# Performance work log

Hardware: AMD Instinct MI355X
Metric: run time of the kernel (lower is better)

## Reference

```python
import math
import jax, jax.numpy as jnp
import numpy as np

B, T, C = 1, 2048, 2048
H, G, D = 16, 4, 128          # n_head, n_query_groups, head_size; C == H*D
Q_PER_KV = H // G
EPS = 1e-5


def _apply_rope_interleaved(x, cos, sin):
    # x: [B, T, h, D]; cos/sin: [T, D//2]; interleaved (GPT-J) style pairs
    x1 = x[..., 0::2]
    x2 = x[..., 1::2]
    c = cos[None, :, None, :]
    s = sin[None, :, None, :]
    o1 = x1 * c - x2 * s
    o2 = x1 * s + x2 * c
    return jnp.stack([o1, o2], axis=-1).reshape(x.shape)


def setup_inputs() -> dict:
    key = jax.random.key(0)
    k0, k1, k2, k3 = jax.random.split(key, 4)
    x = jax.random.normal(k0, (B, T, C), jnp.float32)
    # rotary cache (standard theta=10000)
    inv_freq = 1.0 / (10000.0 ** (np.arange(0, D, 2, dtype=np.float64) / D))
    ang = np.outer(np.arange(T, dtype=np.float64), inv_freq)
    cos = jnp.asarray(np.cos(ang), jnp.float32)
    sin = jnp.asarray(np.sin(ang), jnp.float32)
    # RetNet per-head decay mask: D[h,i,j] = gamma_h^(i-j) for i>=j else 0
    gammas = 1.0 - 2.0 ** (-5.0 - np.arange(H, dtype=np.float64))
    i = np.arange(T)[:, None]
    j = np.arange(T)[None, :]
    diff = np.maximum(i - j, 0).astype(np.float64)
    m = np.where(i >= j, gammas[:, None, None] ** diff[None], 0.0)
    mask = jnp.asarray(m, jnp.float32)
    std = 0.02
    W_reten = jax.random.normal(k1, (C, (H + 2 * G) * D), jnp.float32) * std
    W_gate = jax.random.normal(k2, (C, C), jnp.float32) * std
    W_proj = jax.random.normal(k3, (C, C), jnp.float32) * std
    return {"x": x, "cos": cos, "sin": sin, "mask": mask,
            "W_reten": W_reten, "W_gate": W_gate, "W_proj": W_proj,
            "max_seq_length": T}


def reference(x, cos, sin, mask, W_reten, W_gate, W_proj, max_seq_length):
    # fused qkv projection, grouped-query layout
    qkv = (x @ W_reten).reshape(B, T, G, Q_PER_KV + 2, D)
    q = qkv[..., :Q_PER_KV, :].reshape(B, T, H, D)
    k = qkv[..., Q_PER_KV:Q_PER_KV + 1, :].reshape(B, T, G, D)
    v = qkv[..., Q_PER_KV + 1:, :].reshape(B, T, G, D)
    q = _apply_rope_interleaved(q, cos, sin)
    k = _apply_rope_interleaved(k, cos, sin)
    # [B, h, T, D]
    q = q.transpose(0, 2, 1, 3)
    k = jnp.repeat(k.transpose(0, 2, 1, 3), Q_PER_KV, axis=1)
    v = jnp.repeat(v.transpose(0, 2, 1, 3), Q_PER_KV, axis=1)
    # parallel retention: masked (decay) scores, no softmax
    scale = 1.0 / math.sqrt(D)
    qk = jnp.einsum('bhtd,bhsd->bhts', q, k) * scale
    qk = qk * mask[None]
    y = jnp.einsum('bhts,bhsd->bhtd', qk, v)
    # group norm = RMSNorm (no weight) over head_size
    y = y.transpose(0, 2, 1, 3)  # [B, T, H, D]
    y = y * jax.lax.rsqrt(jnp.mean(y * y, axis=-1, keepdims=True) + EPS)
    y = y.reshape(B, T, C)
    g = jax.nn.silu(x @ W_gate)
    return (g * y) @ W_proj
```

## Files before the change

### kernel.cpp

```cpp
#include <hip/hip_runtime.h>
#include <hip/hip_bf16.h>
#include <cstdint>
#include <cstddef>

typedef __bf16 bf16x8 __attribute__((ext_vector_type(8)));
typedef __bf16 bf16x4 __attribute__((ext_vector_type(4)));
typedef __bf16 bf16x2 __attribute__((ext_vector_type(2)));
typedef float  f32x4  __attribute__((ext_vector_type(4)));
typedef float  f32x2  __attribute__((ext_vector_type(2)));

#define T_SEQ 2048
#define CDIM  2048
#define NH    16
#define NG    4
#define DH    128
#define NCHUNK 32

__device__ __forceinline__ void gl_lds16(const __bf16* g, __bf16* l) {
  __builtin_amdgcn_global_load_lds(
      (const __attribute__((address_space(1))) void*)g,
      (__attribute__((address_space(3))) void*)l, 16, 0, 0);
}

__global__ __launch_bounds__(256) void pre_kernel(
    const float* __restrict__ x, const float* __restrict__ Wr,
    const float* __restrict__ Wg, const float* __restrict__ Wp,
    __bf16* __restrict__ xb, __bf16* __restrict__ wtb, __bf16* __restrict__ wpb) {
  __shared__ __bf16 tile[64][68];
  int bid = blockIdx.x;
  int tid = threadIdx.x;
  if (bid < 2048) {
    size_t i = ((size_t)bid * 256 + tid) * 8;
    f32x4 a = *(const f32x4*)(x + i);
    f32x4 b = *(const f32x4*)(x + i + 4);
    bf16x8 o;
#pragma unroll
    for (int j = 0; j < 4; ++j) { o[j] = (__bf16)a[j]; o[4 + j] = (__bf16)b[j]; }
    *(bf16x8*)(xb + i) = o;
    return;
  }
  int rel = bid - 2048;
  const float* W; __bf16* Wt; int N;
  if (rel < 1536)      { W = Wr; Wt = wtb;                        N = 3072; }
  else if (rel < 2560) { W = Wg; Wt = wtb + (size_t)3072 * CDIM;  N = 2048; rel -= 1536; }
  else                 { W = Wp; Wt = wpb;                        N = 2048; rel -= 2560; }
  const int K = 2048;
  int k0 = (rel & 31) * 64, n0 = (rel >> 5) * 64;
  int c4 = (tid & 15) * 4, r = tid >> 4;
#pragma unroll
  for (int rr = 0; rr < 4; ++rr) {
    int row = r + rr * 16;
    f32x4 v = *(const f32x4*)(W + (size_t)(k0 + row) * N + n0 + c4);
#pragma unroll
    for (int j = 0; j < 4; ++j) tile[row][c4 + j] = (__bf16)v[j];
  }
  __syncthreads();
  int n = tid >> 2, seg = tid & 3;
  __bf16 vals[16];
#pragma unroll
  for (int j = 0; j < 16; ++j) vals[j] = tile[seg * 16 + j][n];
  __bf16* dst = Wt + (size_t)(n0 + n) * K + k0 + seg * 16;
  *(bf16x8*)(dst)     = *(bf16x8*)(&vals[0]);
  *(bf16x8*)(dst + 8) = *(bf16x8*)(&vals[8]);
}

__global__ __launch_bounds__(256) void uscan_kernel(const __bf16* __restrict__ vtb,
                                                    const __bf16* __restrict__ ktb,
                                                    __bf16* __restrict__ St) {
  int bid = blockIdx.x;
  int h = bid >> 4, m = (bid >> 1) & 7, half = bid & 1;
  int g = h >> 2;
  int tid = threadIdx.x, w = tid >> 6, l = tid & 63, lr = l & 15, lg = l >> 4;
  int jf = half * 4 + w;
  float l2g = log2f(1.0f - exp2f(-5.0f - (float)h));
  float ginv = exp2f(-l2g);
  float df   = exp2f(l2g * 64.0f);
  float wk[2];
#pragma unroll
  for (int kk = 0; kk < 2; ++kk) wk[kk] = exp2f(l2g * (float)(64 - (kk * 32 + lg * 8)));
  const __bf16* vrow = vtb + ((size_t)g * DH + m * 16 + lr) * T_SEQ;
  const __bf16* krow = ktb + ((size_t)g * DH + jf * 16 + lr) * T_SEQ;
  f32x4 S = {0.f, 0.f, 0.f, 0.f};
  for (int c = 0; c < NCHUNK; ++c) {
    f32x4 u = {0.f, 0.f, 0.f, 0.f};
#pragma unroll
    for (int kk = 0; kk < 2; ++kk) {
      int j0 = c * 64 + kk * 32 + lg * 8;
      bf16x8 av = *(const bf16x8*)(vrow + j0);
      bf16x8 bv = *(const bf16x8*)(krow + j0);
      bf16x8 aw;
      float wj = wk[kk];
#pragma unroll
      for (int jj = 0; jj < 8; ++jj) { aw[jj] = (__bf16)((float)av[jj] * wj); wj *= ginv; }
      u = __builtin_amdgcn_mfma_f32_16x16x32_bf16(aw, bv, u, 0, 0, 0);
    }
    __bf16* out = St + ((size_t)(h * NCHUNK + c) * 128 + m * 16 + lg * 4) * 128 + jf * 16 + lr;
#pragma unroll
    for (int r = 0; r < 4; ++r) out[r * 128] = (__bf16)S[r];
#pragma unroll
    for (int r = 0; r < 4; ++r) S[r] = df * S[r] + u[r];
  }
}

__global__ __launch_bounds__(256) void attn2_kernel(const __bf16* __restrict__ qb,
    const __bf16* __restrict__ kb, const __bf16* __restrict__ vtb,
    const __bf16* __restrict__ St, const __bf16* __restrict__ gateb,
    __bf16* __restrict__ ynormb) {
  __shared__ __bf16 kl[64 * 128];
  __shared__ __bf16 vl[128 * 64];
  __shared__ __bf16 pl[4][16 * 64];
  int h = blockIdx.x >> 5, qt = blockIdx.x & 31;
  int g = h >> 2;
  int w = threadIdx.x >> 6, l = threadIdx.x & 63;
  int lr = l & 15, lg = l >> 4;
  int t0b = qt * 64;
  int t0 = t0b + w * 16;
  bf16x8 qf[4];
#pragma unroll
  for (int kbk = 0; kbk < 4; ++kbk)
    qf[kbk] = *(const bf16x8*)(qb + ((size_t)h * T_SEQ + t0 + lr) * DH + kbk * 32 + lg * 8);
  float gamma = 1.0f - exp2f(-5.0f - (float)h);
  float l2g = log2f(gamma);
  const float scale = 0.088388347648318447f;
  int s0 = t0b;
#pragma unroll
  for (int it = 0; it < 4; ++it) {
    int fg = it * 256 + threadIdx.x;
    {
      int ss = fg >> 4, gr = fg & 15;
      bf16x8 kv = *(const bf16x8*)(kb + ((size_t)g * T_SEQ + s0 + ss) * DH + gr * 8);
      *(bf16x8*)((char*)kl + ss * 256 + ((gr * 16) ^ ((ss & 7) << 4))) = kv;
    }
    {
      int d = fg >> 3, gv = fg & 7;
      bf16x8 vv = *(const bf16x8*)(vtb + ((size_t)g * DH + d) * T_SEQ + s0 + gv * 8);
      *(bf16x8*)((char*)vl + d * 128 + ((gv * 16) ^ ((d & 7) << 4))) = vv;
    }
  }
  float wfac = scale * exp2f(l2g * (float)(w * 16 + lr));
  bf16x8 qwf[4];
#pragma unroll
  for (int kbk = 0; kbk < 4; ++kbk)
#pragma unroll
    for (int e = 0; e < 8; ++e) qwf[kbk][e] = (__bf16)((float)qf[kbk][e] * wfac);
  f32x4 acc[8] = {};
  const __bf16* Sb = St + (size_t)(h * NCHUNK + qt) * 16384;
#pragma unroll
  for (int dc = 0; dc < 8; ++dc)
#pragma unroll
    for (int kc = 0; kc < 4; ++kc) {
      bf16x8 sf = *(const bf16x8*)(Sb + (dc * 16 + lr) * 128 + kc * 32 + lg * 8);
      acc[dc] = __builtin_amdgcn_mfma_f32_16x16x32_bf16(qwf[kc], sf, acc[dc], 0, 0, 0);
    }
  __syncthreads();
#pragma unroll
  for (int sc = 0; sc < 4; ++sc) {
    f32x4 p = {0.f, 0.f, 0.f, 0.f};
    int srow = sc * 16 + lr;
#pragma unroll
    for (int kbk = 0; kbk < 4; ++kbk) {
      bf16x8 kf = *(const bf16x8*)((char*)kl + srow * 256 +
                                   ((kbk * 64 + lg * 16) ^ ((srow & 7) << 4)));
      p = __builtin_amdgcn_mfma_f32_16x16x32_bf16(qf[kbk], kf, p, 0, 0, 0);
    }
#pragma unroll
    for (int r = 0; r < 4; ++r) {
      int tl = lg * 4 + r;
      int diff = (w * 16 + tl) - srow;
      float val = 0.0f;
      if (diff >= 0) val = p[r] * scale * exp2f((float)diff * l2g);
      *(__bf16*)((char*)(pl[w]) + tl * 128 +
                 (((sc * 16 + lr) * 2) ^ ((tl & 7) << 4))) = (__bf16)val;
    }
  }
  bf16x8 pa[2];
#pragma unroll
  for (int kc = 0; kc < 2; ++kc)
    pa[kc] = *(const bf16x8*)((char*)(pl[w]) + lr * 128 +
                              ((kc * 64 + lg * 16) ^ ((lr & 7) << 4)));
#pragma unroll
  for (int dc = 0; dc < 8; ++dc) {
#pragma unroll
    for (int kc = 0; kc < 2; ++kc) {
      int vrow = dc * 16 + lr;
      bf16x8 vf = *(const bf16x8*)((char*)vl + vrow * 128 +
                                   ((kc * 64 + lg * 16) ^ ((vrow & 7) << 4)));
      acc[dc] = __builtin_amdgcn_mfma_f32_16x16x32_bf16(pa[kc], vf, acc[dc], 0, 0, 0);
    }
  }
  float rs[4];
#pragma unroll
  for (int r = 0; r < 4; ++r) {
    float ssum = 0.f;
#pragma unroll
    for (int dc = 0; dc < 8; ++dc) ssum += acc[dc][r] * acc[dc][r];
    ssum += __shfl_xor(ssum, 1, 64);
    ssum += __shfl_xor(ssum, 2, 64);
    ssum += __shfl_xor(ssum, 4, 64);
    ssum += __shfl_xor(ssum, 8, 64);
    rs[r] = rsqrtf(ssum * (1.0f / 128.0f) + 1e-5f);
  }
#pragma unroll
  for (int dc = 0; dc < 8; ++dc)
#pragma unroll
    for (int r = 0; r < 4; ++r) {
      size_t idx = (size_t)(t0 + lg * 4 + r) * CDIM + h * DH + dc * 16 + lr;
      float gv = (float)gateb[idx];
      ynormb[idx] = (__bf16)(acc[dc][r] * rs[r] * gv);
    }
}

template<int MODE>
__global__ __launch_bounds__(256) void gemm_gl_kernel(
    const __bf16* __restrict__ A, const __bf16* __restrict__ Bt,
    float* __restrict__ Cf, __bf16* __restrict__ Cg,
    const float* __restrict__ cosb, const float* __restrict__ sinb,
    __bf16* __restrict__ qb, __bf16* __restrict__ kb,
    __bf16* __restrict__ vtb, __bf16* __restrict__ ktb,
    int M, int N, int K) {
  __shared__ __bf16 Asb[2 * 64 * 64];
  __shared__ __bf16 Bsb[2 * 128 * 64];
  int m0 = blockIdx.x * 64, n0 = blockIdx.y * 128;
  int tid = threadIdx.x;
  int w = tid >> 6, l = tid & 63;
  int wr = w >> 1, wc = w & 1;
  int lr = l & 15, lg = l >> 4;
  int nk = K >> 6;
  const __bf16* Ab = A + (size_t)m0 * K;
  const __bf16* Bb = Bt + (size_t)n0 * K;
  f32x4 acc[2][4] = {};

  auto stage = [&](int buf, int k0) {
#pragma unroll
    for (int c = 0; c < 2; ++c) {
      int ca = c * 256 + tid, row = ca >> 3, ks = ca & 7;
      gl_lds16(Ab + (size_t)row * K + k0 + ((ks ^ (row & 7)) << 3),
               Asb + buf * 4096 + ca * 8);
    }
#pragma unroll
    for (int c = 0; c < 4; ++c) {
      int cb2 = c * 256 + tid, row = cb2 >> 3, ks = cb2 & 7;
      gl_lds16(Bb + (size_t)row * K + k0 + ((ks ^ (row & 7)) << 3),
               Bsb + buf * 8192 + cb2 * 8);
    }
  };

  stage(0, 0);
  if (nk > 1) {
    stage(1, 64);
    asm volatile("s_waitcnt vmcnt(6)" ::: "memory");
  } else {
    asm volatile("s_waitcnt vmcnt(0)" ::: "memory");
  }
  __builtin_amdgcn_s_barrier();

  int cur = 0;
  for (int kt = 0; kt < nk; ++kt) {
    const char* As = (const char*)(Asb + cur * 4096);
    const char* Bs = (const char*)(Bsb + cur * 8192);
    bf16x8 av[2][2], bv[4][2];
#pragma unroll
    for (int i = 0; i < 2; ++i)
#pragma unroll
      for (int kk = 0; kk < 2; ++kk) {
        int row = wr * 32 + i * 16 + lr;
        av[i][kk] = *(const bf16x8*)(As +
            ((row * 128 + kk * 64 + lg * 16) ^ ((lr & 7) << 4)));
      }
#pragma unroll
    for (int j = 0; j < 4; ++j)
#pragma unroll
      for (int kk = 0; kk < 2; ++kk) {
        int row = wc * 64 + j * 16 + lr;
        bv[j][kk] = *(const bf16x8*)(Bs +
            ((row * 128 + kk * 64 + lg * 16) ^ ((lr & 7) << 4)));
      }
#pragma unroll
    for (int kk = 0; kk < 2; ++kk)
#pragma unroll
      for (int i = 0; i < 2; ++i)
#pragma unroll
        for (int j = 0; j < 4; ++j)
          acc[i][j] = __builtin_amdgcn_mfma_f32_16x16x32_bf16(av[i][kk], bv[j][kk],
                                                              acc[i][j], 0, 0, 0);
    if (kt + 1 < nk) {
      __builtin_amdgcn_s_barrier();
      if (kt + 2 < nk) {
        stage(cur, (kt + 2) << 6);
        asm volatile("s_waitcnt vmcnt(6)" ::: "memory");
      } else {
        asm volatile("s_waitcnt vmcnt(0)" ::: "memory");
      }
      __builtin_amdgcn_s_barrier();
    }
    cur ^= 1;
  }

  if (MODE == 0) {
#pragma unroll
    for (int i = 0; i < 2; ++i) {
      int row = m0 + wr * 32 + i * 16 + lg * 4;
#pragma unroll
      for (int j = 0; j < 4; ++j) {
        int col = n0 + wc * 64 + j * 16 + lr;
#pragma unroll
        for (int r = 0; r < 4; ++r)
          Cf[(size_t)(row + r) * N + col] = acc[i][j][r];
      }
    }
    return;
  }
  if (n0 >= 3072) {
#pragma unroll
    for (int i = 0; i < 2; ++i) {
      int row = m0 + wr * 32 + i * 16 + lg * 4;
#pragma unroll
      for (int j = 0; j < 4; ++j) {
        int col = n0 + wc * 64 + j * 16 + lr;
#pragma unroll
        for (int r = 0; r < 4; ++r) {
          float z = acc[i][j][r];
          float sv = z / (1.0f + expf(-z));
          Cg[(size_t)(row + r) * 2048 + (col - 3072)] = (__bf16)sv;
        }
      }
    }
    return;
  }
#pragma unroll
  for (int i = 0; i < 2; ++i) {
    int row0 = m0 + wr * 32 + i * 16 + lg * 4;
#pragma unroll
    for (int j = 0; j < 4; ++j) {
      int cb = n0 + wc * 64 + j * 16;
      int g = cb / 768, cm = cb % 768;
      int dbase = (cm < 512) ? (cm & 127) : (cm < 640) ? (cm - 512) : (cm - 640);
      int d = dbase + lr;
      float ov[4];
      if (cm < 640) {
#pragma unroll
        for (int r = 0; r < 4; ++r) {
          float z = acc[i][j][r];
          float pz = __shfl_xor(z, 1, 64);
          int t = row0 + r;
          float cc = cosb[t * 64 + (d >> 1)];
          float ss = sinb[t * 64 + (d >> 1)];
          ov[r] = (lr & 1) ? (pz * ss + z * cc) : (z * cc - pz * ss);
        }
      } else {
#pragma unroll
        for (int r = 0; r < 4; ++r) ov[r] = acc[i][j][r];
      }
      if (cm < 512) {
        int hh = g * 4 + (cm >> 7);
#pragma unroll
        for (int r = 0; r < 4; ++r)
          qb[((size_t)hh * T_SEQ + row0 + r) * DH + d] = (__bf16)ov[r];
      } else if (cm < 640) {
        bf16x4 kv;
#pragma unroll
        for (int r = 0; r < 4; ++r) {
          kv[r] = (__bf16)ov[r];
          kb[((size_t)g * T_SEQ + row0 + r) * DH + d] = kv[r];
        }
        *(bf16x4*)(ktb + ((size_t)g * DH + d) * T_SEQ + row0) = kv;
      } else {
        bf16x4 vv;
#pragma unroll
        for (int r = 0; r < 4; ++r) vv[r] = (__bf16)ov[r];
        *(bf16x4*)(vtb + ((size_t)g * DH + d) * T_SEQ + row0) = vv;
      }
    }
  }
}

extern "C" void kernel_launch(void* const* d_in, const int* in_sizes, int n_in,
                              void* d_out, int out_size, void* d_ws, size_t ws_size,
                              hipStream_t stream) {
  const float* x    = (const float*)d_in[0];
  const float* cosb = (const float*)d_in[1];
  const float* sinb = (const float*)d_in[2];
  const float* Wr   = (const float*)d_in[4];
  const float* Wg   = (const float*)d_in[5];
  const float* Wp   = (const float*)d_in[6];

  char* ws = (char*)d_ws;
  size_t off = 0;
  auto alloc = [&](size_t bytes) { void* p = ws + off; off += (bytes + 255) & ~(size_t)255; return p; };
  __bf16* xb     = (__bf16*)alloc((size_t)CDIM * CDIM * 2);
  __bf16* wtb    = (__bf16*)alloc((size_t)5120 * CDIM * 2);
  __bf16* wpb    = (__bf16*)alloc((size_t)CDIM * CDIM * 2);
  __bf16* qb     = (__bf16*)alloc((size_t)NH * T_SEQ * DH * 2);
  __bf16* kbp    = (__bf16*)alloc((size_t)NG * T_SEQ * DH * 2);
  __bf16* vtb    = (__bf16*)alloc((size_t)NG * DH * T_SEQ * 2);
  __bf16* ktb    = (__bf16*)alloc((size_t)NG * DH * T_SEQ * 2);
  __bf16* gateb  = (__bf16*)alloc((size_t)CDIM * CDIM * 2);
  __bf16* Stb    = (__bf16*)alloc((size_t)NH * NCHUNK * 128 * 128 * 2);
  __bf16* ynormb = (__bf16*)alloc((size_t)T_SEQ * CDIM * 2);

  pre_kernel<<<5632, 256, 0, stream>>>(x, Wr, Wg, Wp, xb, wtb, wpb);
  gemm_gl_kernel<1><<<dim3(32, 40), 256, 0, stream>>>(
      xb, wtb, nullptr, gateb, cosb, sinb, qb, kbp, vtb, ktb, 2048, 5120, 2048);
  uscan_kernel<<<256, 256, 0, stream>>>(vtb, ktb, Stb);
  attn2_kernel<<<NH * NCHUNK, 256, 0, stream>>>(qb, kbp, vtb, Stb, gateb, ynormb);
  gemm_gl_kernel<0><<<dim3(32, 16), 256, 0, stream>>>(
      ynormb, wpb, (float*)d_out, nullptr, nullptr, nullptr, nullptr, nullptr, nullptr, nullptr,
      2048, 2048, 2048);
}
```

Before: 156.4 us.

## Prefetch scan loads, vectorize gated epilogue via LDS, swizzle GEMM block order

```diff
diff --git a/kernel.cpp b/kernel.cpp
--- a/kernel.cpp
+++ b/kernel.cpp
@@ -81,18 +81,31 @@
   const __bf16* vrow = vtb + ((size_t)g * DH + m * 16 + lr) * T_SEQ;
   const __bf16* krow = ktb + ((size_t)g * DH + jf * 16 + lr) * T_SEQ;
   f32x4 S = {0.f, 0.f, 0.f, 0.f};
+  bf16x8 pav[2], pbv[2];
+#pragma unroll
+  for (int kk = 0; kk < 2; ++kk) {
+    int j0 = kk * 32 + lg * 8;
+    pav[kk] = *(const bf16x8*)(vrow + j0);
+    pbv[kk] = *(const bf16x8*)(krow + j0);
+  }
   for (int c = 0; c < NCHUNK; ++c) {
+    bf16x8 cav[2] = {pav[0], pav[1]}, cbv[2] = {pbv[0], pbv[1]};
+    if (c + 1 < NCHUNK) {
+#pragma unroll
+      for (int kk = 0; kk < 2; ++kk) {
+        int j0 = (c + 1) * 64 + kk * 32 + lg * 8;
+        pav[kk] = *(const bf16x8*)(vrow + j0);
+        pbv[kk] = *(const bf16x8*)(krow + j0);
+      }
+    }
     f32x4 u = {0.f, 0.f, 0.f, 0.f};
 #pragma unroll
     for (int kk = 0; kk < 2; ++kk) {
-      int j0 = c * 64 + kk * 32 + lg * 8;
-      bf16x8 av = *(const bf16x8*)(vrow + j0);
-      bf16x8 bv = *(const bf16x8*)(krow + j0);
       bf16x8 aw;
       float wj = wk[kk];
 #pragma unroll
-      for (int jj = 0; jj < 8; ++jj) { aw[jj] = (__bf16)((float)av[jj] * wj); wj *= ginv; }
-      u = __builtin_amdgcn_mfma_f32_16x16x32_bf16(aw, bv, u, 0, 0, 0);
+      for (int jj = 0; jj < 8; ++jj) { aw[jj] = (__bf16)((float)cav[kk][jj] * wj); wj *= ginv; }
+      u = __builtin_amdgcn_mfma_f32_16x16x32_bf16(aw, cbv[kk], u, 0, 0, 0);
     }
     __bf16* out = St + ((size_t)(h * NCHUNK + c) * 128 + m * 16 + lg * 4) * 128 + jf * 16 + lr;
 #pragma unroll
@@ -200,14 +213,27 @@
     ssum += __shfl_xor(ssum, 8, 64);
     rs[r] = rsqrtf(ssum * (1.0f / 128.0f) + 1e-5f);
   }
+  __syncthreads();
 #pragma unroll
   for (int dc = 0; dc < 8; ++dc)
 #pragma unroll
     for (int r = 0; r < 4; ++r) {
-      size_t idx = (size_t)(t0 + lg * 4 + r) * CDIM + h * DH + dc * 16 + lr;
-      float gv = (float)gateb[idx];
-      ynormb[idx] = (__bf16)(acc[dc][r] * rs[r] * gv);
-    }
+      int lrow = w * 16 + lg * 4 + r;
+      *(__bf16*)((char*)kl + lrow * 256 + (((dc * 16 + lr) * 2) ^ ((lrow & 7) << 4)))
+          = (__bf16)(acc[dc][r] * rs[r]);
+    }
+#pragma unroll
+  for (int p = 0; p < 4; ++p) {
+    int lrow = w * 16 + p * 4 + (l >> 4);
+    int col0 = (l & 15) * 8;
+    bf16x8 yv = *(const bf16x8*)((char*)kl + lrow * 256 + ((col0 * 2) ^ ((lrow & 7) << 4)));
+    size_t idx = (size_t)(t0b + lrow) * CDIM + h * DH + col0;
+    bf16x8 gv = *(const bf16x8*)(gateb + idx);
+    bf16x8 ov;
+#pragma unroll
+    for (int j = 0; j < 8; ++j) ov[j] = (__bf16)((float)yv[j] * (float)gv[j]);
+    *(bf16x8*)(ynormb + idx) = ov;
+  }
 }
 
 template<int MODE>
@@ -220,7 +246,11 @@
     int M, int N, int K) {
   __shared__ __bf16 Asb[2 * 64 * 64];
   __shared__ __bf16 Bsb[2 * 128 * 64];
-  int m0 = blockIdx.x * 64, n0 = blockIdx.y * 128;
+  int nwgx = gridDim.x;
+  int lin = blockIdx.y * nwgx + blockIdx.x;
+  int nwg = nwgx * gridDim.y;
+  int swz = (lin & 7) * (nwg >> 3) + (lin >> 3);
+  int m0 = (swz % nwgx) * 64, n0 = (swz / nwgx) * 128;
   int tid = threadIdx.x;
   int w = tid >> 6, l = tid & 63;
   int wr = w >> 1, wc = w & 1;
```

After: 160.8 us. 1.03x slower.
